# Kernel tuning notes

Hardware: AMD Instinct MI355X
Metric: run time of the kernel (lower is better)

Reference implementation:

```python
import jax, jax.numpy as jnp
import numpy as np

T, B, E, H = 2048, 2, 1024, 16

def setup_inputs() -> dict:
    rng = jax.random.key(0)
    ks = jax.random.split(rng, 7)
    s = 0.02
    return {
        "query": jax.random.normal(ks[0], (T, B, E), jnp.float32),
        "key": jax.random.normal(ks[1], (T, B, E), jnp.float32),
        "value": jax.random.normal(ks[2], (T, B, E), jnp.float32),
        "in_proj_weight": jax.random.normal(ks[3], (3 * E, E), jnp.float32) * s,
        "in_proj_bias": jax.random.normal(ks[4], (3 * E,), jnp.float32) * s,
        "out_proj_weight": jax.random.normal(ks[5], (E, E), jnp.float32) * s,
        "out_proj_bias": jax.random.normal(ks[6], (E,), jnp.float32) * s,
    }

def reference(query, key, value, in_proj_weight, in_proj_bias, out_proj_weight, out_proj_bias):
    tgt_len, bsz, embed_dim = query.shape
    num_heads = H
    head_dim = embed_dim // num_heads
    scaling = head_dim ** -0.5
    wq, wk, wv = jnp.split(in_proj_weight, 3, axis=0)
    bq, bk, bv = jnp.split(in_proj_bias, 3, axis=0)
    # projections: F.linear(x, W, b) = x @ W.T + b
    q = (query @ wq.T + bq) * scaling          # (T, B, E)
    k = key @ wk.T + bk                        # (S, B, E)
    v = value @ wv.T + bv                      # (S, B, E)
    # (len, B, E) -> (B*H, len, head_dim), matching torch view+transpose
    def to_heads(x):
        L = x.shape[0]
        return x.reshape(L, bsz * num_heads, head_dim).transpose(1, 0, 2)
    q, k, v = to_heads(q), to_heads(k), to_heads(v)
    scores = jnp.einsum('bqd,bkd->bqk', q, k)  # (B*H, T, S)
    attn = jax.nn.softmax(scores, axis=-1)
    out = jnp.einsum('bqk,bkd->bqd', attn, v)  # (B*H, T, head_dim)
    out = out.transpose(1, 0, 2).reshape(tgt_len, bsz, embed_dim)
    out = out @ out_proj_weight.T + out_proj_bias
    return out
```

## Files before the change

kernel.cpp:

```cpp
#include <hip/hip_runtime.h>
#include <cstdint>
#include <cstddef>

#define QSCALE 0.18033688011112042f

typedef __attribute__((ext_vector_type(8))) short bf16x8;
typedef __attribute__((ext_vector_type(4))) float f32x4;

#define MFMA(a, b, c) __builtin_amdgcn_mfma_f32_16x16x32_bf16(a, b, c, 0, 0, 0)

typedef union { unsigned int u[4]; bf16x8 b; } pku;

__device__ __forceinline__ unsigned short cvt_bf16(float x) {
  union { float f; unsigned int u; } v;
  v.f = x;
  unsigned int r = v.u + 0x7FFFu + ((v.u >> 16) & 1u);
  return (unsigned short)(r >> 16);
}

__device__ __forceinline__ void gll16(const void* g, void* l) {
  __builtin_amdgcn_global_load_lds(
      (const __attribute__((address_space(1))) unsigned int*)g,
      (__attribute__((address_space(3))) unsigned int*)l, 16, 0, 0);
}

__device__ __forceinline__ unsigned int pack_bf16(float lo, float hi) {
  union { float f; unsigned int u; } a, b;
  a.f = lo; b.f = hi;
  return __builtin_amdgcn_perm(b.u + 0x8000u, a.u + 0x8000u, 0x07060302u);
}

__global__ void cvt_all(const float* __restrict__ q,
                        const float* __restrict__ k,
                        const float* __restrict__ v,
                        const float* __restrict__ ipw,
                        const float* __restrict__ opw,
                        unsigned short* __restrict__ dst) {
  const size_t i = ((size_t)blockIdx.x * 256 + threadIdx.x) * 8;
  const float* src;
  float scale = 1.0f;
  if (i < 4194304) src = q + i;
  else if (i < 8388608) src = k + (i - 4194304);
  else if (i < 12582912) src = v + (i - 8388608);
  else {
    const size_t w = i - 12582912;
    if (w < 3145728) { src = ipw + w; if (w < 1048576) scale = QSCALE; }
    else src = opw + (w - 3145728);
  }
  float4 a = *(const float4*)src;
  float4 b = *(const float4*)(src + 4);
  uint4 o;
  o.x = cvt_bf16(a.x * scale) | ((unsigned int)cvt_bf16(a.y * scale) << 16);
  o.y = cvt_bf16(a.z * scale) | ((unsigned int)cvt_bf16(a.w * scale) << 16);
  o.z = cvt_bf16(b.x * scale) | ((unsigned int)cvt_bf16(b.y * scale) << 16);
  o.w = cvt_bf16(b.z * scale) | ((unsigned int)cvt_bf16(b.w * scale) << 16);
  *(uint4*)(dst + i) = o;
}

__global__ __launch_bounds__(256, 3) void gemm_qkv(
    const unsigned short* __restrict__ X,
    const unsigned short* __restrict__ W,
    const float* __restrict__ bias,
    unsigned short* __restrict__ Qh,
    unsigned short* __restrict__ Kh,
    unsigned short* __restrict__ Vt)
{
  __shared__ unsigned short As[128 * 32];
  __shared__ unsigned short Bs[128 * 32];
  const int tid = threadIdx.x;
  const int wave = tid >> 6, lane = tid & 63;
  const int quad = lane >> 4, l16 = lane & 15;
  const int z = blockIdx.z;
  const int m0 = blockIdx.y * 128;
  const int n0 = blockIdx.x * 128;
  const unsigned short* Ab = X + (size_t)z * 4194304 + (size_t)m0 * 1024;
  const unsigned short* Bb = W + ((size_t)z * 1024 + n0) * 1024;
  const int wr = (wave >> 1) * 64, wc = (wave & 1) * 64;

  const f32x4 z4 = {0.f, 0.f, 0.f, 0.f};
  f32x4 acc[4][4];
#pragma unroll
  for (int i = 0; i < 4; ++i)
#pragma unroll
    for (int j = 0; j < 4; ++j) acc[i][j] = z4;

  const int c0 = wave * 128 + lane;
  for (int k0 = 0; k0 < 1024; k0 += 32) {
    __syncthreads();
#pragma unroll
    for (int j = 0; j < 2; ++j) {
      const int c = c0 + j * 64;
      const int row = c >> 2, kc = c & 3;
      gll16(Ab + (size_t)row * 1024 + k0 + kc * 8, &As[c * 8]);
      gll16(Bb + (size_t)row * 1024 + k0 + kc * 8, &Bs[c * 8]);
    }
    __syncthreads();
    bf16x8 af[4], bfr[4];
#pragma unroll
    for (int rt = 0; rt < 4; ++rt)
      af[rt] = *(const bf16x8*)&As[(wr + rt * 16 + l16) * 32 + quad * 8];
#pragma unroll
    for (int ct = 0; ct < 4; ++ct)
      bfr[ct] = *(const bf16x8*)&Bs[(wc + ct * 16 + l16) * 32 + quad * 8];
#pragma unroll
    for (int rt = 0; rt < 4; ++rt)
#pragma unroll
      for (int ct = 0; ct < 4; ++ct)
        acc[rt][ct] = MFMA(af[rt], bfr[ct], acc[rt][ct]);
  }

#pragma unroll
  for (int rt = 0; rt < 4; ++rt)
#pragma unroll
    for (int ct = 0; ct < 4; ++ct) {
      const int gn = n0 + wc + ct * 16 + l16;
      float bv = bias[z * 1024 + gn];
      if (z == 0) bv *= QSCALE;
      const int h = gn >> 6, d = gn & 63;
#pragma unroll
      for (int r = 0; r < 4; ++r) {
        const int gm = m0 + wr + rt * 16 + quad * 4 + r;
        const int t = gm >> 1, b = gm & 1;
        const int bh = b * 16 + h;
        const unsigned short o = cvt_bf16(acc[rt][ct][r] + bv);
        if (z == 0)      Qh[((size_t)bh * 2048 + t) * 64 + d] = o;
        else if (z == 1) Kh[((size_t)bh * 2048 + t) * 64 + d] = o;
        else             Vt[((size_t)bh * 64 + d) * 2048 + t] = o;
      }
    }
}

__global__ __launch_bounds__(256, 2) void attn(
    const unsigned short* __restrict__ Qh,
    const unsigned short* __restrict__ Kh,
    const unsigned short* __restrict__ Vt,
    unsigned short* __restrict__ O)
{
  __shared__ unsigned short Ks[128 * 64];
  __shared__ unsigned short Vs[64 * 128];
  const int tid = threadIdx.x;
  const int wave = tid >> 6, lane = tid & 63;
  const int quad = lane >> 4, l16 = lane & 15;
  const int qt = blockIdx.x, bh = blockIdx.y;
  const unsigned short* Qb = Qh + ((size_t)bh * 2048 + qt * 128 + wave * 32) * 64;
  const unsigned short* Kb = Kh + (size_t)bh * 2048 * 64;
  const unsigned short* Vb = Vt + (size_t)bh * 64 * 2048;

  bf16x8 qf[2][2];
#pragma unroll
  for (int rt = 0; rt < 2; ++rt)
#pragma unroll
    for (int kk = 0; kk < 2; ++kk)
      qf[rt][kk] = *(const bf16x8*)(Qb + (size_t)(rt * 16 + l16) * 64 + kk * 32 + quad * 8);

  const f32x4 z4 = {0.f, 0.f, 0.f, 0.f};
  f32x4 oacc[2][4];
  f32x4 lacc[2] = {z4, z4};
#pragma unroll
  for (int rt = 0; rt < 2; ++rt)
#pragma unroll
    for (int c = 0; c < 4; ++c) oacc[rt][c] = z4;

#pragma unroll 1
  for (int it = 0; it < 16; ++it) {
    const int s0 = it * 128;
    __syncthreads();
#pragma unroll
    for (int j = 0; j < 4; ++j) {
      const int c = wave * 256 + j * 64 + lane;
      const int r = c >> 3, cc = c & 7;
      gll16(Kb + (size_t)(s0 + r) * 64 + (cc ^ (r & 7)) * 8, &Ks[c * 8]);
      const int r2 = c >> 4, cc2 = c & 15;
      gll16(Vb + (size_t)r2 * 2048 + s0 + (cc2 ^ (r2 & 15)) * 8, &Vs[c * 8]);
    }
    __syncthreads();

    unsigned int pkl[2][8], pkh[2][8];
#pragma unroll
    for (int ct = 0; ct < 8; ++ct) {
      f32x4 s0v = z4, s1v = z4;
#pragma unroll
      for (int kk = 0; kk < 2; ++kk) {
        const int R = ct * 16 + l16;
        const int phys = (kk * 4 + quad) ^ (R & 7);
        const bf16x8 kfr = *(const bf16x8*)&Ks[R * 64 + phys * 8];
        s0v = MFMA(kfr, qf[0][kk], s0v);
        s1v = MFMA(kfr, qf[1][kk], s1v);
      }
      f32x4 p0, p1;
#pragma unroll
      for (int r = 0; r < 4; ++r) { p0[r] = exp2f(s0v[r]); p1[r] = exp2f(s1v[r]); }
      lacc[0] += p0;
      lacc[1] += p1;
      pkl[0][ct] = pack_bf16(p0[0], p0[1]);
      pkh[0][ct] = pack_bf16(p0[2], p0[3]);
      pkl[1][ct] = pack_bf16(p1[0], p1[1]);
      pkh[1][ct] = pack_bf16(p1[2], p1[3]);
    }

#pragma unroll
    for (int kk2 = 0; kk2 < 4; ++kk2) {
      pku a0, a1;
      a0.u[0] = pkl[0][kk2 * 2];     a0.u[1] = pkh[0][kk2 * 2];
      a0.u[2] = pkl[0][kk2 * 2 + 1]; a0.u[3] = pkh[0][kk2 * 2 + 1];
      a1.u[0] = pkl[1][kk2 * 2];     a1.u[1] = pkh[1][kk2 * 2];
      a1.u[2] = pkl[1][kk2 * 2 + 1]; a1.u[3] = pkh[1][kk2 * 2 + 1];
      const int lcA = (kk2 * 8 + quad) ^ (l16 << 1);
      const int lcB = (kk2 * 8 + 4 + quad) ^ (l16 << 1);
#pragma unroll
      for (int ctd = 0; ctd < 4; ++ctd) {
        const int R = ctd * 16 + l16;
        pku vv;
        *(uint2*)&vv.u[0] = *(const uint2*)&Vs[R * 128 + lcA * 4];
        *(uint2*)&vv.u[2] = *(const uint2*)&Vs[R * 128 + lcB * 4];
        oacc[0][ctd] = MFMA(a0.b, vv.b, oacc[0][ctd]);
        oacc[1][ctd] = MFMA(a1.b, vv.b, oacc[1][ctd]);
      }
    }
  }

  const int b = bh >> 4, h = bh & 15;
#pragma unroll
  for (int rt = 0; rt < 2; ++rt) {
    float hs = lacc[rt][0] + lacc[rt][1] + lacc[rt][2] + lacc[rt][3];
    hs += __shfl_xor(hs, 16);
    hs += __shfl_xor(hs, 32);
#pragma unroll
    for (int r = 0; r < 4; ++r) {
      const float lv = __shfl(hs, quad * 4 + r, 64);
      const float inv = 1.0f / lv;
      const int t = qt * 128 + wave * 32 + rt * 16 + quad * 4 + r;
#pragma unroll
      for (int ctd = 0; ctd < 4; ++ctd) {
        const int col = h * 64 + ctd * 16 + l16;
        O[((size_t)t * 2 + b) * 1024 + col] = cvt_bf16(oacc[rt][ctd][r] * inv);
      }
    }
  }
}

__global__ __launch_bounds__(256, 4) void gemm_out(
    const unsigned short* __restrict__ A,
    const unsigned short* __restrict__ W,
    const float* __restrict__ bias,
    float* __restrict__ out)
{
  __shared__ unsigned short As[128 * 32];
  __shared__ unsigned short Bs[64 * 32];
  const int tid = threadIdx.x;
  const int wave = tid >> 6, lane = tid & 63;
  const int quad = lane >> 4, l16 = lane & 15;
  const int m0 = blockIdx.y * 128;
  const int n0 = blockIdx.x * 64;
  const unsigned short* Ab = A + (size_t)m0 * 1024;
  const unsigned short* Bb = W + (size_t)n0 * 1024;
  const int wr = (wave >> 1) * 64, wc = (wave & 1) * 32;

  const f32x4 z4 = {0.f, 0.f, 0.f, 0.f};
  f32x4 acc[4][2];
#pragma unroll
  for (int i = 0; i < 4; ++i)
#pragma unroll
    for (int j = 0; j < 2; ++j) acc[i][j] = z4;

  for (int k0 = 0; k0 < 1024; k0 += 32) {
    __syncthreads();
#pragma unroll
    for (int j = 0; j < 3; ++j) {
      const int c = j * 256 + tid;
      if (j < 2) {
        const int row = c >> 2, kc = c & 3;
        gll16(Ab + (size_t)row * 1024 + k0 + kc * 8, &As[c * 8]);
      } else {
        const int bc = c - 512;
        const int row = bc >> 2, kc = bc & 3;
        gll16(Bb + (size_t)row * 1024 + k0 + kc * 8, &Bs[bc * 8]);
      }
    }
    __syncthreads();
    bf16x8 af[4], bfr[2];
#pragma unroll
    for (int rt = 0; rt < 4; ++rt)
      af[rt] = *(const bf16x8*)&As[(wr + rt * 16 + l16) * 32 + quad * 8];
#pragma unroll
    for (int ct = 0; ct < 2; ++ct)
      bfr[ct] = *(const bf16x8*)&Bs[(wc + ct * 16 + l16) * 32 + quad * 8];
#pragma unroll
    for (int rt = 0; rt < 4; ++rt)
#pragma unroll
      for (int ct = 0; ct < 2; ++ct)
        acc[rt][ct] = MFMA(af[rt], bfr[ct], acc[rt][ct]);
  }

#pragma unroll
  for (int rt = 0; rt < 4; ++rt)
#pragma unroll
    for (int ct = 0; ct < 2; ++ct) {
      const int gn = n0 + wc + ct * 16 + l16;
      const float bv = bias[gn];
#pragma unroll
      for (int r = 0; r < 4; ++r) {
        const int gm = m0 + wr + rt * 16 + quad * 4 + r;
        out[(size_t)gm * 1024 + gn] = acc[rt][ct][r] + bv;
      }
    }
}

extern "C" void kernel_launch(void* const* d_in, const int* in_sizes, int n_in,
                              void* d_out, int out_size, void* d_ws, size_t ws_size,
                              hipStream_t stream) {
  const float* q   = (const float*)d_in[0];
  const float* k   = (const float*)d_in[1];
  const float* v   = (const float*)d_in[2];
  const float* ipw = (const float*)d_in[3];
  const float* ipb = (const float*)d_in[4];
  const float* opw = (const float*)d_in[5];
  const float* opb = (const float*)d_in[6];

  unsigned short* ws = (unsigned short*)d_ws;
  unsigned short* X  = ws;
  unsigned short* Wb = ws + 12582912;
  unsigned short* Wo = ws + 15728640;
  unsigned short* Qh = ws + 16777216;
  unsigned short* Kh = ws + 20971520;
  unsigned short* Vx = ws + 25165824;
  unsigned short* Oa = ws + 29360128;

  cvt_all<<<dim3(8192), 256, 0, stream>>>(q, k, v, ipw, opw, ws);
  gemm_qkv<<<dim3(8, 32, 3), 256, 0, stream>>>(X, Wb, ipb, Qh, Kh, Vx);
  attn<<<dim3(16, 32), 256, 0, stream>>>(Qh, Kh, Vx, Oa);
  gemm_out<<<dim3(16, 32), 256, 0, stream>>>(Oa, Wo, opb, (float*)d_out);
}
```

Before: 238.1 us.

## Permute V layout for single 16B LDS reads, compute row sums via MFMA

```diff
diff --git a/kernel.cpp b/kernel.cpp
--- a/kernel.cpp
+++ b/kernel.cpp
@@ -22,6 +22,14 @@
   __builtin_amdgcn_global_load_lds(
       (const __attribute__((address_space(1))) unsigned int*)g,
       (__attribute__((address_space(3))) unsigned int*)l, 16, 0, 0);
+}
+
+__device__ __forceinline__ float fast_exp2(float x) {
+#if __has_builtin(__builtin_amdgcn_exp2f)
+  return __builtin_amdgcn_exp2f(x);
+#else
+  float r; asm("v_exp_f32 %0, %1" : "=v"(r) : "v"(x)); return r;
+#endif
 }
 
 __device__ __forceinline__ unsigned int pack_bf16(float lo, float hi) {
@@ -125,7 +133,11 @@
         const unsigned short o = cvt_bf16(acc[rt][ct][r] + bv);
         if (z == 0)      Qh[((size_t)bh * 2048 + t) * 64 + d] = o;
         else if (z == 1) Kh[((size_t)bh * 2048 + t) * 64 + d] = o;
-        else             Vt[((size_t)bh * 64 + d) * 2048 + t] = o;
+        else {
+          const int w32 = t & 31;
+          const int tp = (t & ~31) | (((w32 >> 2) & 3) << 3) | ((w32 >> 4) << 2) | (w32 & 3);
+          Vt[((size_t)bh * 64 + d) * 2048 + tp] = o;
+        }
       }
     }
 }
@@ -153,6 +165,24 @@
     for (int kk = 0; kk < 2; ++kk)
       qf[rt][kk] = *(const bf16x8*)(Qb + (size_t)(rt * 16 + l16) * 64 + kk * 32 + quad * 8);
 
+  const unsigned short* kp[4];
+  const unsigned short* vp[4];
+  unsigned short* kl[4];
+  unsigned short* vl[4];
+#pragma unroll
+  for (int j = 0; j < 4; ++j) {
+    const int c = wave * 256 + j * 64 + lane;
+    const int r = c >> 3, cc = c & 7;
+    kp[j] = Kb + (size_t)r * 64 + (cc ^ (r & 7)) * 8;
+    kl[j] = &Ks[c * 8];
+    const int r2 = c >> 4, cc2 = c & 15;
+    vp[j] = Vb + (size_t)r2 * 2048 + (cc2 ^ (r2 & 15)) * 8;
+    vl[j] = &Vs[c * 8];
+  }
+
+  pku ones;
+  ones.u[0] = ones.u[1] = ones.u[2] = ones.u[3] = 0x3F803F80u;
+
   const f32x4 z4 = {0.f, 0.f, 0.f, 0.f};
   f32x4 oacc[2][4];
   f32x4 lacc[2] = {z4, z4};
@@ -163,19 +193,17 @@
 
 #pragma unroll 1
   for (int it = 0; it < 16; ++it) {
-    const int s0 = it * 128;
     __syncthreads();
 #pragma unroll
     for (int j = 0; j < 4; ++j) {
-      const int c = wave * 256 + j * 64 + lane;
-      const int r = c >> 3, cc = c & 7;
-      gll16(Kb + (size_t)(s0 + r) * 64 + (cc ^ (r & 7)) * 8, &Ks[c * 8]);
-      const int r2 = c >> 4, cc2 = c & 15;
-      gll16(Vb + (size_t)r2 * 2048 + s0 + (cc2 ^ (r2 & 15)) * 8, &Vs[c * 8]);
-    }
-    __syncthreads();
-
-    unsigned int pkl[2][8], pkh[2][8];
+      gll16(kp[j], kl[j]);
+      gll16(vp[j], vl[j]);
+      kp[j] += 128 * 64;
+      vp[j] += 128;
+    }
+    __syncthreads();
+
+    unsigned int pkl_[2][8], pkh_[2][8];
 #pragma unroll
     for (int ct = 0; ct < 8; ++ct) {
       f32x4 s0v = z4, s1v = z4;
@@ -189,46 +217,39 @@
       }
       f32x4 p0, p1;
 #pragma unroll
-      for (int r = 0; r < 4; ++r) { p0[r] = exp2f(s0v[r]); p1[r] = exp2f(s1v[r]); }
-      lacc[0] += p0;
-      lacc[1] += p1;
-      pkl[0][ct] = pack_bf16(p0[0], p0[1]);
-      pkh[0][ct] = pack_bf16(p0[2], p0[3]);
-      pkl[1][ct] = pack_bf16(p1[0], p1[1]);
-      pkh[1][ct] = pack_bf16(p1[2], p1[3]);
+      for (int r = 0; r < 4; ++r) { p0[r] = fast_exp2(s0v[r]); p1[r] = fast_exp2(s1v[r]); }
+      pkl_[0][ct] = pack_bf16(p0[0], p0[1]);
+      pkh_[0][ct] = pack_bf16(p0[2], p0[3]);
+      pkl_[1][ct] = pack_bf16(p1[0], p1[1]);
+      pkh_[1][ct] = pack_bf16(p1[2], p1[3]);
     }
 
 #pragma unroll
     for (int kk2 = 0; kk2 < 4; ++kk2) {
       pku a0, a1;
-      a0.u[0] = pkl[0][kk2 * 2];     a0.u[1] = pkh[0][kk2 * 2];
-      a0.u[2] = pkl[0][kk2 * 2 + 1]; a0.u[3] = pkh[0][kk2 * 2 + 1];
-      a1.u[0] = pkl[1][kk2 * 2];     a1.u[1] = pkh[1][kk2 * 2];
-      a1.u[2] = pkl[1][kk2 * 2 + 1]; a1.u[3] = pkh[1][kk2 * 2 + 1];
-      const int lcA = (kk2 * 8 + quad) ^ (l16 << 1);
-      const int lcB = (kk2 * 8 + 4 + quad) ^ (l16 << 1);
+      a0.u[0] = pkl_[0][kk2 * 2];     a0.u[1] = pkh_[0][kk2 * 2];
+      a0.u[2] = pkl_[0][kk2 * 2 + 1]; a0.u[3] = pkh_[0][kk2 * 2 + 1];
+      a1.u[0] = pkl_[1][kk2 * 2];     a1.u[1] = pkh_[1][kk2 * 2];
+      a1.u[2] = pkl_[1][kk2 * 2 + 1]; a1.u[3] = pkh_[1][kk2 * 2 + 1];
 #pragma unroll
       for (int ctd = 0; ctd < 4; ++ctd) {
         const int R = ctd * 16 + l16;
-        pku vv;
-        *(uint2*)&vv.u[0] = *(const uint2*)&Vs[R * 128 + lcA * 4];
-        *(uint2*)&vv.u[2] = *(const uint2*)&Vs[R * 128 + lcB * 4];
-        oacc[0][ctd] = MFMA(a0.b, vv.b, oacc[0][ctd]);
-        oacc[1][ctd] = MFMA(a1.b, vv.b, oacc[1][ctd]);
-      }
+        const int phys = (kk2 * 4 + quad) ^ (R & 15);
+        const bf16x8 vv = *(const bf16x8*)&Vs[R * 128 + phys * 8];
+        oacc[0][ctd] = MFMA(a0.b, vv, oacc[0][ctd]);
+        oacc[1][ctd] = MFMA(a1.b, vv, oacc[1][ctd]);
+      }
+      lacc[0] = MFMA(a0.b, ones.b, lacc[0]);
+      lacc[1] = MFMA(a1.b, ones.b, lacc[1]);
     }
   }
 
   const int b = bh >> 4, h = bh & 15;
 #pragma unroll
-  for (int rt = 0; rt < 2; ++rt) {
-    float hs = lacc[rt][0] + lacc[rt][1] + lacc[rt][2] + lacc[rt][3];
-    hs += __shfl_xor(hs, 16);
-    hs += __shfl_xor(hs, 32);
+  for (int rt = 0; rt < 2; ++rt)
 #pragma unroll
     for (int r = 0; r < 4; ++r) {
-      const float lv = __shfl(hs, quad * 4 + r, 64);
-      const float inv = 1.0f / lv;
+      const float inv = 1.0f / lacc[rt][r];
       const int t = qt * 128 + wave * 32 + rt * 16 + quad * 4 + r;
 #pragma unroll
       for (int ctd = 0; ctd < 4; ++ctd) {
@@ -236,7 +257,6 @@
         O[((size_t)t * 2 + b) * 1024 + col] = cvt_bf16(oacc[rt][ctd][r] * inv);
       }
     }
-  }
 }
 
 __global__ __launch_bounds__(256, 4) void gemm_out(
```

Measured after the change: 216.3 us. 9.2% less time.
